# Kernel optimization log

Measured on AMD Instinct MI355X. Metric: run time of the kernel, lower is better.

## Reference

```python
import jax, jax.numpy as jnp
import numpy as np

N, M_CTX, SIN, YDIM, SPROJ = 16384, 4096, 256, 7, 256


def setup_inputs() -> dict:
    key = jax.random.key(0)
    k1, k2, k3, k4, k5 = jax.random.split(key, 5)
    return {
        "x": jax.random.normal(k1, (N, SIN), dtype=jnp.float32),
        "y": jax.random.normal(k2, (M_CTX, YDIM), dtype=jnp.float32),
        "Wq": jax.random.normal(k3, (SIN, SPROJ), dtype=jnp.float32) / np.sqrt(SIN),
        "Wk": jax.random.normal(k4, (YDIM, SPROJ), dtype=jnp.float32) / np.sqrt(YDIM),
        "Wv": jax.random.normal(k5, (YDIM, SPROJ), dtype=jnp.float32) / np.sqrt(YDIM),
    }


def smooth_softmax(x):
    # softmax over keys (axis=1) blended with 0.1*relu, renormalized
    s = jax.nn.softmax(x, axis=1)
    num = jax.nn.relu(x) * 0.1 + s
    return num / jnp.sum(num, axis=1, keepdims=True)


def reference(x, y, Wq, Wk, Wv):
    XQ = x @ Wq            # [N, P]
    YK = y @ Wk            # [M, P]
    YV = y @ Wv            # [M, P]
    scores = (XQ @ YK.T) / jnp.sqrt(jnp.asarray(YK.shape[1], XQ.dtype))  # [N, M]
    A = smooth_softmax(scores)
    return A @ YV          # [N, P]
```

## Files before the change

### kernel.cpp

```cpp
#include <hip/hip_runtime.h>
#include <hip/hip_bf16.h>

#define N_Q   16384
#define MCTX  4096
#define DSIN  256
#define YDIM  7
#define PDIM  256
#define BK    32

typedef __attribute__((ext_vector_type(8))) short s16x8;
typedef __attribute__((ext_vector_type(4))) float f32x4;
typedef unsigned short u16;

static __device__ __forceinline__ u16 f2bf(float f) {
    union { float f; unsigned u; } v; v.f = f;
    unsigned r = v.u + 0x7fffu + ((v.u >> 16) & 1u);
    return (u16)(r >> 16);
}
static __device__ __forceinline__ float bf2f(u16 h) {
    union { unsigned u; float f; } v; v.u = ((unsigned)h) << 16;
    return v.f;
}
static __device__ __forceinline__ unsigned pk2bf(float lo, float hi) {
    __hip_bfloat162 h2 = __float22bfloat162_rn(make_float2(lo, hi));
    union { __hip_bfloat162 h; unsigned u; } v; v.h = h2;
    return v.u;
}
static __device__ __forceinline__ u16 f2bf_hw(float f) {
    __hip_bfloat16 h = __float2bfloat16(f);
    union { __hip_bfloat16 h; u16 u; } v; v.h = h;
    return v.u;
}
static __device__ __forceinline__ f32x4 mfma16(s16x8 a, s16x8 b, f32x4 c) {
    return __builtin_amdgcn_mfma_f32_16x16x32_bf16(a, b, c, 0, 0, 0);
}
static __device__ __forceinline__ void gload_lds16(const u16* g, u16* l) {
    __builtin_amdgcn_global_load_lds(
        (const __attribute__((address_space(1))) unsigned int*)(g),
        (__attribute__((address_space(3))) unsigned int*)(l), 16, 0, 0);
}

__global__ void k_prep(const float* __restrict__ Wq, u16* __restrict__ WtH,
                       u16* __restrict__ WtL, const float* __restrict__ y,
                       const float* __restrict__ Wk, const float* __restrict__ Wv,
                       u16* __restrict__ YK, u16* __restrict__ YVb) {
    if (blockIdx.x < PDIM) {
        int n = blockIdx.x;
        int k = threadIdx.x;
        float w = Wq[(size_t)k * PDIM + n];
        u16 h = f2bf(w);
        WtH[(size_t)n * DSIN + k] = h;
        WtL[(size_t)n * DSIN + k] = f2bf(w - bf2f(h));
    } else {
        int kb = blockIdx.x - PDIM;
        int p  = threadIdx.x;
        float wk[YDIM], wv[YDIM];
#pragma unroll
        for (int j = 0; j < YDIM; ++j) {
            wk[j] = Wk[(size_t)j * PDIM + p];
            wv[j] = Wv[(size_t)j * PDIM + p];
        }
        u16 vbuf[32];
#pragma unroll
        for (int m = 0; m < 32; ++m) {
            int key = kb * 32 + m;
            float ak = 0.f, av = 0.f;
#pragma unroll
            for (int j = 0; j < YDIM; ++j) {
                float yy = y[(size_t)key * YDIM + j];
                ak += yy * wk[j];
                av += yy * wv[j];
            }
            YK[(size_t)key * PDIM + p] = f2bf(ak * 0.0625f);
            vbuf[m] = f2bf(av);
        }
        s16x8* dst = (s16x8*)(YVb + ((size_t)kb * PDIM + p) * 32);
#pragma unroll
        for (int c = 0; c < 4; ++c) dst[c] = ((s16x8*)vbuf)[c];
    }
}

__global__ __launch_bounds__(256, 2) void k_xq(const float* __restrict__ x,
                                               const u16* __restrict__ WtH,
                                               const u16* __restrict__ WtL,
                                               u16* __restrict__ XQ) {
    __shared__ u16 xH[32 * 256];
    __shared__ u16 xL[32 * 256];
    const int tid = threadIdx.x;
    const int rowg0 = blockIdx.x * 32;
#pragma unroll
    for (int i = 0; i < 4; ++i) {
        int row = (tid >> 5) + i * 8;
        int c32 = tid & 31;
        const float* px = x + (size_t)(rowg0 + row) * DSIN + c32 * 8;
        float4 a = *(const float4*)px;
        float4 b = *(const float4*)(px + 4);
        float vals[8] = {a.x, a.y, a.z, a.w, b.x, b.y, b.z, b.w};
        s16x8 h, l;
#pragma unroll
        for (int j = 0; j < 8; ++j) {
            u16 hh = f2bf(vals[j]);
            h[j] = (short)hh;
            l[j] = (short)f2bf(vals[j] - bf2f(hh));
        }
        int pc = c32 ^ (row & 7);
        *(s16x8*)(xH + row * 256 + pc * 8) = h;
        *(s16x8*)(xL + row * 256 + pc * 8) = l;
    }
    __syncthreads();

    const int wave = tid >> 6, lane = tid & 63;
    const int quad = lane >> 4, m16 = lane & 15;
    const int rh = wave & 1, ph = wave >> 1;
    const int rowl = rh * 16 + m16;
    const int swz = rowl & 7;
    s16x8 ah[8], al[8];
#pragma unroll
    for (int kf = 0; kf < 8; ++kf) {
        int pc = (kf * 4 + quad) ^ swz;
        ah[kf] = *(const s16x8*)(xH + rowl * 256 + pc * 8);
        al[kf] = *(const s16x8*)(xL + rowl * 256 + pc * 8);
    }
#pragma unroll
    for (int ptl = 0; ptl < 8; ++ptl) {
        int pt = ph * 8 + ptl;
        f32x4 acc = (f32x4){0.f, 0.f, 0.f, 0.f};
#pragma unroll
        for (int kf = 0; kf < 8; ++kf) {
            size_t idx = (size_t)(pt * 16 + m16) * DSIN + kf * 32 + quad * 8;
            s16x8 bh = *(const s16x8*)(WtH + idx);
            s16x8 bl = *(const s16x8*)(WtL + idx);
            acc = mfma16(ah[kf], bh, acc);
            acc = mfma16(al[kf], bh, acc);
            acc = mfma16(ah[kf], bl, acc);
        }
#pragma unroll
        for (int r = 0; r < 4; ++r)
            XQ[(size_t)(rowg0 + rh * 16 + quad * 4 + r) * PDIM + pt * 16 + m16] =
                f2bf(acc[r]);
    }
}

__global__ __launch_bounds__(256, 2) void k_attn(const u16* __restrict__ XQ,
                                                 const u16* __restrict__ YK,
                                                 const u16* __restrict__ YVb,
                                                 u16* __restrict__ accE,
                                                 u16* __restrict__ accR,
                                                 float* __restrict__ lsum,
                                                 float* __restrict__ rsum,
                                                 int msPerSplit) {
    __shared__ u16 Kt[32 * 256];
    __shared__ u16 Pe[64 * 40];
    __shared__ u16 Pr[64 * 40];

    const int tid = threadIdx.x;
    const int wave = tid >> 6, lane = tid & 63;
    const int quad = lane >> 4, m16 = lane & 15;
    const int split = blockIdx.y;
    const int qbase = blockIdx.x * 64;
    const int key_begin = split * msPerSplit;
    const int iters = msPerSplit / BK;
    const int pslice = wave * 64;
    const int kr0 = m16 + m16;
    const int swz0 = kr0 & 7;

    s16x8 qf[8];
    const u16* qp = XQ + (size_t)(qbase + wave * 16 + m16) * DSIN;
#pragma unroll
    for (int kf = 0; kf < 8; ++kf)
        qf[kf] = *(const s16x8*)(qp + kf * 32 + quad * 8);

    f32x4 aE[4][4], aR[4][4];
#pragma unroll
    for (int g = 0; g < 4; ++g)
#pragma unroll
        for (int t = 0; t < 4; ++t) {
            aE[g][t] = (f32x4){0.f, 0.f, 0.f, 0.f};
            aR[g][t] = (f32x4){0.f, 0.f, 0.f, 0.f};
        }
    float lacc[4] = {0.f, 0.f, 0.f, 0.f}, racc[4] = {0.f, 0.f, 0.f, 0.f};

    auto stage = [&](int key0) {
#pragma unroll
        for (int c = 0; c < 4; ++c) {
            int l = (wave * 4 + c) * 64 + lane;
            int r = l >> 5;
            int sc = (l & 31) ^ (r & 7);
            gload_lds16(YK + (size_t)(key0 + r) * DSIN + sc * 8,
                        Kt + (size_t)(wave * 4 + c) * 512);
        }
    };
    stage(key_begin);

    for (int it = 0; it < iters; ++it) {
        const int key0 = key_begin + it * BK;
        __syncthreads();

        f32x4 s0 = (f32x4){0.f, 0.f, 0.f, 0.f};
        f32x4 s1 = (f32x4){0.f, 0.f, 0.f, 0.f};
        __builtin_amdgcn_s_setprio(1);
#pragma unroll
        for (int kf = 0; kf < 8; ++kf) {
            int pc0 = (kf * 4 + quad) ^ swz0;
            int pc1 = pc0 ^ 1;
            s16x8 b0 = *(const s16x8*)(Kt + kr0 * 256 + pc0 * 8);
            s16x8 b1 = *(const s16x8*)(Kt + (kr0 + 1) * 256 + pc1 * 8);
            s0 = mfma16(qf[kf], b0, s0);
            s1 = mfma16(qf[kf], b1, s1);
        }
        __builtin_amdgcn_s_setprio(0);
#pragma unroll
        for (int r = 0; r < 4; ++r) {
            float e0 = __expf(s0[r]), e1 = __expf(s1[r]);
            float rl0 = fmaxf(s0[r], 0.f), rl1 = fmaxf(s1[r], 0.f);
            lacc[r] += e0 + e1;
            racc[r] += rl0 + rl1;
            int row = wave * 16 + quad * 4 + r;
            *(unsigned*)(Pe + row * 40 + kr0) = pk2bf(e0, e1);
            *(unsigned*)(Pr + row * 40 + kr0) = pk2bf(rl0, rl1);
        }
        __syncthreads();

        s16x8 vf[4];
        const u16* vb = YVb + (size_t)((key0 >> 5) * PDIM) * 32;
#pragma unroll
        for (int t = 0; t < 4; ++t)
            vf[t] = *(const s16x8*)(vb + (size_t)(pslice + t * 16 + m16) * 32 + quad * 8);

        if (it + 1 < iters) stage(key0 + BK);

        __builtin_amdgcn_s_setprio(1);
#pragma unroll
        for (int g = 0; g < 4; ++g) {
            s16x8 pa = *(const s16x8*)(Pe + (g * 16 + m16) * 40 + quad * 8);
            s16x8 pb = *(const s16x8*)(Pr + (g * 16 + m16) * 40 + quad * 8);
#pragma unroll
            for (int t = 0; t < 4; ++t) {
                aE[g][t] = mfma16(pa, vf[t], aE[g][t]);
                aR[g][t] = mfma16(pb, vf[t], aR[g][t]);
            }
        }
        __builtin_amdgcn_s_setprio(0);
    }

    size_t ob = ((size_t)split * N_Q + qbase) * PDIM;
#pragma unroll
    for (int g = 0; g < 4; ++g)
#pragma unroll
        for (int t = 0; t < 4; ++t)
#pragma unroll
            for (int r = 0; r < 4; ++r) {
                size_t o = ob + (size_t)(g * 16 + quad * 4 + r) * PDIM + pslice + t * 16 + m16;
                accE[o] = f2bf_hw(aE[g][t][r]);
                accR[o] = f2bf_hw(aR[g][t][r]);
            }
#pragma unroll
    for (int r = 0; r < 4; ++r) {
        lacc[r] += __shfl_xor(lacc[r], 1);
        lacc[r] += __shfl_xor(lacc[r], 2);
        lacc[r] += __shfl_xor(lacc[r], 4);
        lacc[r] += __shfl_xor(lacc[r], 8);
        racc[r] += __shfl_xor(racc[r], 1);
        racc[r] += __shfl_xor(racc[r], 2);
        racc[r] += __shfl_xor(racc[r], 4);
        racc[r] += __shfl_xor(racc[r], 8);
    }
    if (m16 < 4) {
        float lv = (m16 == 0) ? lacc[0] : (m16 == 1) ? lacc[1] : (m16 == 2) ? lacc[2] : lacc[3];
        float rv = (m16 == 0) ? racc[0] : (m16 == 1) ? racc[1] : (m16 == 2) ? racc[2] : racc[3];
        int row = split * N_Q + qbase + wave * 16 + quad * 4 + m16;
        lsum[row] = lv;
        rsum[row] = rv;
    }
}

__global__ void k_comb(const u16* __restrict__ accE, const u16* __restrict__ accR,
                       const float* __restrict__ lsum, const float* __restrict__ rsum,
                       float* __restrict__ out, int nsplit) {
    int row = blockIdx.x * 8 + (threadIdx.x >> 5);
    int col = (threadIdx.x & 31) * 8;
    size_t idx = (size_t)row * PDIM + col;
    const size_t NP = (size_t)N_Q * PDIM;
    float E[8] = {0.f, 0.f, 0.f, 0.f, 0.f, 0.f, 0.f, 0.f};
    float R[8] = {0.f, 0.f, 0.f, 0.f, 0.f, 0.f, 0.f, 0.f};
    float L = 0.f, Rs = 0.f;
    for (int s = 0; s < nsplit; ++s) {
        s16x8 e = *(const s16x8*)(accE + s * NP + idx);
        s16x8 r = *(const s16x8*)(accR + s * NP + idx);
#pragma unroll
        for (int j = 0; j < 8; ++j) {
            E[j] += bf2f((u16)e[j]);
            R[j] += bf2f((u16)r[j]);
        }
        L  += lsum[(size_t)s * N_Q + row];
        Rs += rsum[(size_t)s * N_Q + row];
    }
    float invL = 1.f / L, invD = 1.f / (1.f + 0.1f * Rs);
    float4 o0, o1;
    o0.x = (0.1f * R[0] + E[0] * invL) * invD;
    o0.y = (0.1f * R[1] + E[1] * invL) * invD;
    o0.z = (0.1f * R[2] + E[2] * invL) * invD;
    o0.w = (0.1f * R[3] + E[3] * invL) * invD;
    o1.x = (0.1f * R[4] + E[4] * invL) * invD;
    o1.y = (0.1f * R[5] + E[5] * invL) * invD;
    o1.z = (0.1f * R[6] + E[6] * invL) * invD;
    o1.w = (0.1f * R[7] + E[7] * invL) * invD;
    *(float4*)(out + idx) = o0;
    *(float4*)(out + idx + 4) = o1;
}

extern "C" void kernel_launch(void* const* d_in, const int* in_sizes, int n_in,
                              void* d_out, int out_size, void* d_ws, size_t ws_size,
                              hipStream_t stream) {
    const float* x  = (const float*)d_in[0];
    const float* y  = (const float*)d_in[1];
    const float* Wq = (const float*)d_in[2];
    const float* Wk = (const float*)d_in[3];
    const float* Wv = (const float*)d_in[4];
    float* out = (float*)d_out;

    char* ws = (char*)d_ws;
    size_t off = 0;
    auto take = [&](size_t bytes) -> char* {
        char* p = ws + off;
        off += (bytes + 255) & ~(size_t)255;
        return p;
    };
    u16* XQ  = (u16*)take((size_t)N_Q * PDIM * 2);
    u16* WtH = (u16*)take((size_t)PDIM * DSIN * 2);
    u16* WtL = (u16*)take((size_t)PDIM * DSIN * 2);
    u16* YK  = (u16*)take((size_t)MCTX * PDIM * 2);
    u16* YVb = (u16*)take((size_t)MCTX * PDIM * 2);

    size_t perSplit = (size_t)N_Q * PDIM * 2 * 2 + (size_t)N_Q * 4 * 2 + 1024;
    int nsplit = (ws_size >= off + 2 * perSplit + 4096) ? 2 : 1;

    u16*   accE = (u16*)take((size_t)nsplit * N_Q * PDIM * 2);
    u16*   accR = (u16*)take((size_t)nsplit * N_Q * PDIM * 2);
    float* lsum = (float*)take((size_t)nsplit * N_Q * 4);
    float* rsum = (float*)take((size_t)nsplit * N_Q * 4);

    hipLaunchKernelGGL(k_prep, dim3(PDIM + MCTX/32), dim3(256), 0, stream,
                       Wq, WtH, WtL, y, Wk, Wv, YK, YVb);
    hipLaunchKernelGGL(k_xq,   dim3(N_Q/32), dim3(256), 0, stream, x, WtH, WtL, XQ);
    hipLaunchKernelGGL(k_attn, dim3(N_Q/64, nsplit), dim3(256), 0, stream,
                       XQ, YK, YVb, accE, accR, lsum, rsum, MCTX / nsplit);
    hipLaunchKernelGGL(k_comb, dim3(N_Q/8), dim3(256), 0, stream,
                       accE, accR, lsum, rsum, out, nsplit);
}
```

Measured before the change: 221.8 us.

## Merge XQ projection and K/V projection into one kernel with finer work split

Splits the Wq transpose into its own small kernel and fuses the XQ projection with the YK/YV projection into one launch. XQ blocks are halved along the output dimension (two blocks per 32-row tile), and K/V blocks handle 8 keys instead of 32, giving more blocks and targeting 3 blocks per CU. This is meant to cut launch count and improve load balance and occupancy in the projection stage. In exchange, the x tile is loaded and split into bf16 hi/lo twice per row tile, which duplicates that global read and conversion work.

After: 222.4 us. Within noise of the previous version (+0.3%).

```diff
diff --git a/kernel.cpp b/kernel.cpp
--- a/kernel.cpp
+++ b/kernel.cpp
@@ -40,30 +40,97 @@
         (__attribute__((address_space(3))) unsigned int*)(l), 16, 0, 0);
 }
 
-__global__ void k_prep(const float* __restrict__ Wq, u16* __restrict__ WtH,
-                       u16* __restrict__ WtL, const float* __restrict__ y,
-                       const float* __restrict__ Wk, const float* __restrict__ Wv,
-                       u16* __restrict__ YK, u16* __restrict__ YVb) {
-    if (blockIdx.x < PDIM) {
-        int n = blockIdx.x;
-        int k = threadIdx.x;
-        float w = Wq[(size_t)k * PDIM + n];
-        u16 h = f2bf(w);
-        WtH[(size_t)n * DSIN + k] = h;
-        WtL[(size_t)n * DSIN + k] = f2bf(w - bf2f(h));
+__global__ void k_wt(const float* __restrict__ Wq, u16* __restrict__ WtH,
+                     u16* __restrict__ WtL) {
+    int n = blockIdx.x;
+    int k = threadIdx.x;
+    float w = Wq[(size_t)k * PDIM + n];
+    u16 h = f2bf(w);
+    WtH[(size_t)n * DSIN + k] = h;
+    WtL[(size_t)n * DSIN + k] = f2bf(w - bf2f(h));
+}
+
+__global__ __launch_bounds__(256, 3) void k_main(const float* __restrict__ x,
+                                                 const u16* __restrict__ WtH,
+                                                 const u16* __restrict__ WtL,
+                                                 u16* __restrict__ XQ,
+                                                 const float* __restrict__ y,
+                                                 const float* __restrict__ Wk,
+                                                 const float* __restrict__ Wv,
+                                                 u16* __restrict__ YK,
+                                                 u16* __restrict__ YVb) {
+    __shared__ u16 xH[32 * 256];
+    __shared__ u16 xL[32 * 256];
+    const int bx = blockIdx.x;
+    const int tid = threadIdx.x;
+
+    if (bx < (N_Q / 32) * 2) {
+        const int rowg0 = (bx >> 1) * 32;
+        const int sub = bx & 1;
+#pragma unroll
+        for (int i = 0; i < 4; ++i) {
+            int row = (tid >> 5) + i * 8;
+            int c32 = tid & 31;
+            const float* px = x + (size_t)(rowg0 + row) * DSIN + c32 * 8;
+            float4 a = *(const float4*)px;
+            float4 b = *(const float4*)(px + 4);
+            float vals[8] = {a.x, a.y, a.z, a.w, b.x, b.y, b.z, b.w};
+            s16x8 h, l;
+#pragma unroll
+            for (int j = 0; j < 8; ++j) {
+                u16 hh = f2bf(vals[j]);
+                h[j] = (short)hh;
+                l[j] = (short)f2bf(vals[j] - bf2f(hh));
+            }
+            int pc = c32 ^ (row & 7);
+            *(s16x8*)(xH + row * 256 + pc * 8) = h;
+            *(s16x8*)(xL + row * 256 + pc * 8) = l;
+        }
+        __syncthreads();
+
+        const int wave = tid >> 6, lane = tid & 63;
+        const int quad = lane >> 4, m16 = lane & 15;
+        const int rh = wave & 1, ph = wave >> 1;
+        const int rowl = rh * 16 + m16;
+        const int swz = rowl & 7;
+        s16x8 ah[8], al[8];
+#pragma unroll
+        for (int kf = 0; kf < 8; ++kf) {
+            int pc = (kf * 4 + quad) ^ swz;
+            ah[kf] = *(const s16x8*)(xH + rowl * 256 + pc * 8);
+            al[kf] = *(const s16x8*)(xL + rowl * 256 + pc * 8);
+        }
+#pragma unroll
+        for (int ptl = 0; ptl < 4; ++ptl) {
+            int pt = ph * 8 + sub * 4 + ptl;
+            f32x4 acc = (f32x4){0.f, 0.f, 0.f, 0.f};
+#pragma unroll
+            for (int kf = 0; kf < 8; ++kf) {
+                size_t idx = (size_t)(pt * 16 + m16) * DSIN + kf * 32 + quad * 8;
+                s16x8 bh = *(const s16x8*)(WtH + idx);
+                s16x8 bl = *(const s16x8*)(WtL + idx);
+                acc = mfma16(ah[kf], bh, acc);
+                acc = mfma16(al[kf], bh, acc);
+                acc = mfma16(ah[kf], bl, acc);
+            }
+#pragma unroll
+            for (int r = 0; r < 4; ++r)
+                XQ[(size_t)(rowg0 + rh * 16 + quad * 4 + r) * PDIM + pt * 16 + m16] =
+                    f2bf(acc[r]);
+        }
     } else {
-        int kb = blockIdx.x - PDIM;
-        int p  = threadIdx.x;
+        int kb8 = bx - (N_Q / 32) * 2;
+        int p = tid;
         float wk[YDIM], wv[YDIM];
 #pragma unroll
         for (int j = 0; j < YDIM; ++j) {
             wk[j] = Wk[(size_t)j * PDIM + p];
             wv[j] = Wv[(size_t)j * PDIM + p];
         }
-        u16 vbuf[32];
-#pragma unroll
-        for (int m = 0; m < 32; ++m) {
-            int key = kb * 32 + m;
+        u16 vbuf[8];
+#pragma unroll
+        for (int m = 0; m < 8; ++m) {
+            int key = kb8 * 8 + m;
             float ak = 0.f, av = 0.f;
 #pragma unroll
             for (int j = 0; j < YDIM; ++j) {
@@ -74,70 +141,8 @@
             YK[(size_t)key * PDIM + p] = f2bf(ak * 0.0625f);
             vbuf[m] = f2bf(av);
         }
-        s16x8* dst = (s16x8*)(YVb + ((size_t)kb * PDIM + p) * 32);
-#pragma unroll
-        for (int c = 0; c < 4; ++c) dst[c] = ((s16x8*)vbuf)[c];
-    }
-}
-
-__global__ __launch_bounds__(256, 2) void k_xq(const float* __restrict__ x,
-                                               const u16* __restrict__ WtH,
-                                               const u16* __restrict__ WtL,
-                                               u16* __restrict__ XQ) {
-    __shared__ u16 xH[32 * 256];
-    __shared__ u16 xL[32 * 256];
-    const int tid = threadIdx.x;
-    const int rowg0 = blockIdx.x * 32;
-#pragma unroll
-    for (int i = 0; i < 4; ++i) {
-        int row = (tid >> 5) + i * 8;
-        int c32 = tid & 31;
-        const float* px = x + (size_t)(rowg0 + row) * DSIN + c32 * 8;
-        float4 a = *(const float4*)px;
-        float4 b = *(const float4*)(px + 4);
-        float vals[8] = {a.x, a.y, a.z, a.w, b.x, b.y, b.z, b.w};
-        s16x8 h, l;
-#pragma unroll
-        for (int j = 0; j < 8; ++j) {
-            u16 hh = f2bf(vals[j]);
-            h[j] = (short)hh;
-            l[j] = (short)f2bf(vals[j] - bf2f(hh));
-        }
-        int pc = c32 ^ (row & 7);
-        *(s16x8*)(xH + row * 256 + pc * 8) = h;
-        *(s16x8*)(xL + row * 256 + pc * 8) = l;
-    }
-    __syncthreads();
-
-    const int wave = tid >> 6, lane = tid & 63;
-    const int quad = lane >> 4, m16 = lane & 15;
-    const int rh = wave & 1, ph = wave >> 1;
-    const int rowl = rh * 16 + m16;
-    const int swz = rowl & 7;
-    s16x8 ah[8], al[8];
-#pragma unroll
-    for (int kf = 0; kf < 8; ++kf) {
-        int pc = (kf * 4 + quad) ^ swz;
-        ah[kf] = *(const s16x8*)(xH + rowl * 256 + pc * 8);
-        al[kf] = *(const s16x8*)(xL + rowl * 256 + pc * 8);
-    }
-#pragma unroll
-    for (int ptl = 0; ptl < 8; ++ptl) {
-        int pt = ph * 8 + ptl;
-        f32x4 acc = (f32x4){0.f, 0.f, 0.f, 0.f};
-#pragma unroll
-        for (int kf = 0; kf < 8; ++kf) {
-            size_t idx = (size_t)(pt * 16 + m16) * DSIN + kf * 32 + quad * 8;
-            s16x8 bh = *(const s16x8*)(WtH + idx);
-            s16x8 bl = *(const s16x8*)(WtL + idx);
-            acc = mfma16(ah[kf], bh, acc);
-            acc = mfma16(al[kf], bh, acc);
-            acc = mfma16(ah[kf], bl, acc);
-        }
-#pragma unroll
-        for (int r = 0; r < 4; ++r)
-            XQ[(size_t)(rowg0 + rh * 16 + quad * 4 + r) * PDIM + pt * 16 + m16] =
-                f2bf(acc[r]);
+        *(s16x8*)(YVb + ((size_t)(kb8 >> 2) * PDIM + p) * 32 + (kb8 & 3) * 8) =
+            *(s16x8*)vbuf;
     }
 }
 
@@ -340,9 +345,9 @@
     float* lsum = (float*)take((size_t)nsplit * N_Q * 4);
     float* rsum = (float*)take((size_t)nsplit * N_Q * 4);
 
-    hipLaunchKernelGGL(k_prep, dim3(PDIM + MCTX/32), dim3(256), 0, stream,
-                       Wq, WtH, WtL, y, Wk, Wv, YK, YVb);
-    hipLaunchKernelGGL(k_xq,   dim3(N_Q/32), dim3(256), 0, stream, x, WtH, WtL, XQ);
+    hipLaunchKernelGGL(k_wt,   dim3(PDIM), dim3(DSIN), 0, stream, Wq, WtH, WtL);
+    hipLaunchKernelGGL(k_main, dim3((N_Q/32)*2 + MCTX/8), dim3(256), 0, stream,
+                       x, WtH, WtL, XQ, y, Wk, Wv, YK, YVb);
     hipLaunchKernelGGL(k_attn, dim3(N_Q/64, nsplit), dim3(256), 0, stream,
                        XQ, YK, YVb, accE, accR, lsum, rsum, MCTX / nsplit);
     hipLaunchKernelGGL(k_comb, dim3(N_Q/8), dim3(256), 0, stream,
```
